# Kernel tuning notes

Hardware: AMD Instinct MI355X
Metric: run time of the kernel (lower is better)

## Reference

```python
import jax, jax.numpy as jnp
import numpy as np

N_NODES = 50000
IN_C = 128
OUT_C = 128
EDGE_F = 65
N_EDGES = 800000
EDGE_ATTR_COLS = 70


def setup_inputs() -> dict:
    key = jax.random.key(0)
    ks = jax.random.split(key, 10)
    fcat = 3 * IN_C + EDGE_F
    sc = lambda d: 1.0 / np.sqrt(d)
    return {
        "x": jax.random.normal(ks[0], (N_NODES, IN_C), dtype=jnp.float32),
        "edge_index": jax.random.randint(ks[1], (2, N_EDGES), 0, N_NODES, dtype=jnp.int32),
        "edge_attr": jax.random.normal(ks[2], (N_EDGES, EDGE_ATTR_COLS), dtype=jnp.float32),
        # f_linear: Linear(fcat -> IN_C, bias=True) followed by ELU
        "Wf": jax.random.normal(ks[3], (fcat, IN_C), dtype=jnp.float32) * sc(fcat),
        "bf": jnp.zeros((IN_C,), dtype=jnp.float32),
        # q/k linears: Linear(IN_C -> IN_C, bias=False)
        "Wq": jax.random.normal(ks[4], (IN_C, IN_C), dtype=jnp.float32) * sc(IN_C),
        "Wk": jax.random.normal(ks[5], (IN_C, IN_C), dtype=jnp.float32) * sc(IN_C),
        # alinear: Linear(IN_C -> 1, bias=False) + Tanh
        "Wa": jax.random.normal(ks[6], (IN_C, 1), dtype=jnp.float32) * sc(IN_C),
        # updatalinear: Linear(IN_C -> OUT_C, bias=True)
        "Wu": jax.random.normal(ks[7], (IN_C, OUT_C), dtype=jnp.float32) * sc(IN_C),
        "bu": jnp.zeros((OUT_C,), dtype=jnp.float32),
    }


def reference(x, edge_index, edge_attr, Wf, bf, Wq, Wk, Wa, Wu, bu):
    src = edge_index[0]
    tgt = edge_index[1]
    # message: gather endpoints, concat with delta and edge features, fuse MLP
    ni = x[src]                      # [E, C]
    nj = x[tgt]                      # [E, C]
    mask = (edge_attr[:, 0:1] < 8).astype(x.dtype)  # [E, 1]
    fcat = jnp.concatenate([ni, nj, ni - nj, edge_attr[:, :EDGE_F]], axis=1)
    f = jax.nn.elu(fcat @ Wf + bf) * mask           # [E, C]
    scale = IN_C ** (-0.5)
    q = ni @ Wq                                      # [E, C]
    k = f @ Wk                                       # [E, C]
    a = jnp.tanh((q * k * scale) @ Wa)               # [E, 1]
    # NOTE: faithful to source: denominator = exp(sum(a)), not sum(exp(a))
    numerator = jnp.exp(a)
    a_sum = jax.ops.segment_sum(a, src, num_segments=N_NODES)   # [N, 1]
    denominator = jnp.exp(a_sum)[src]                            # [E, 1]
    s = numerator / denominator
    z = s * f                                        # [E, C]
    # aggregate: scatter-sum over source nodes
    aggr = jax.ops.segment_sum(z, src, num_segments=N_NODES)     # [N, C]
    # update
    return (x + aggr) @ Wu + bu
```

## Files before the change

### kernel.cpp

```cpp
#include <hip/hip_runtime.h>

#define E_EDGES 800000
#define NN 50000
#define C 128
#define EAC 70
#define EF 65
#define NB 196
#define SCALE 0.08838834764831845f

typedef __attribute__((ext_vector_type(8))) short short8;
typedef __attribute__((ext_vector_type(4))) float floatx4;

__device__ __forceinline__ unsigned short f2bf(float f) {
  unsigned u = __builtin_bit_cast(unsigned, f);
  unsigned r = (u + 0x7FFFu + ((u >> 16) & 1u)) >> 16;
  return (unsigned short)r;
}
__device__ __forceinline__ float bf2f(unsigned short h) {
  unsigned u = ((unsigned)h) << 16;
  return __builtin_bit_cast(float, u);
}

__device__ __forceinline__ float fast_tanh(float x) {
  float xc = fminf(fmaxf(x, -15.f), 15.f);
  float t = __expf(2.f * xc);
  return (t - 1.f) * __builtin_amdgcn_rcpf(t + 1.f);
}
__device__ __forceinline__ float fast_elu(float v) {
  return v > 0.f ? v : (__expf(v) - 1.f);
}

__device__ __forceinline__ void atomic_pk_add_bf16(unsigned short* p, float lo, float hi) {
  unsigned pk = (unsigned)f2bf(lo) | ((unsigned)f2bf(hi) << 16);
  asm volatile("global_atomic_pk_add_bf16 %0, %1, off"
               :: "v"((unsigned long long)(uintptr_t)p), "v"(pk) : "memory");
}

__global__ void setup_kernel(const float* __restrict__ Wf, const float* __restrict__ Wq,
                             const float* __restrict__ Wk, const float* __restrict__ Wa,
                             const int* __restrict__ src, unsigned short* __restrict__ wfrag,
                             float* __restrict__ Wm, int* __restrict__ deg) {
  int b = blockIdx.x;
  if (b < 64) {
    int idx = b * 256 + threadIdx.x;
    int r = idx >> 7, d = idx & 127;
    const float* wq = Wq + (size_t)r * C;
    const float* wk = Wk + (size_t)d * C;
    float s = 0.f;
    for (int c = 0; c < C; ++c) s += wq[c] * Wa[c] * wk[c];
    Wm[idx] = s * SCALE;
  } else if (b < 240) {
    int idx = (b - 64) * 256 + threadIdx.x;
    int arr = idx >> 14;
    int rem = idx & 16383;
    int j = rem & 7;
    int l = (rem >> 3) & 63;
    int st = rem >> 9;
    int s = st >> 3, t = st & 7;
    int k = s * 32 + (l >> 4) * 8 + j;
    int n = t * 16 + (l & 15);
    float v;
    if (arr == 0)      v = Wf[k * C + n] + Wf[(256 + k) * C + n];
    else if (arr == 1) v = Wf[(128 + k) * C + n] - Wf[(256 + k) * C + n];
    else               v = (k < EF) ? Wf[(384 + k) * C + n] : 0.f;
    wfrag[idx] = f2bf(v);
  } else {
    int e = (b - 240) * 256 + threadIdx.x;
    atomicAdd(deg + src[e], 1);
  }
}

__global__ __launch_bounds__(256) void m_kernel(const float* __restrict__ x,
                                                const float* __restrict__ Wm,
                                                unsigned short* __restrict__ M,
                                                unsigned short* __restrict__ XB) {
  __shared__ float rows[32][129];
  int b0 = blockIdx.x * 32;
  for (int idx = threadIdx.x; idx < 32 * 128; idx += 256) {
    int r = idx >> 7, i = idx & 127;
    int n = b0 + r;
    float v = 0.f;
    if (n < NN) {
      v = x[(size_t)n * C + i];
      XB[(size_t)n * C + i] = f2bf(v);
    }
    rows[r][i] = v;
  }
  __syncthreads();
  int tr = threadIdx.x >> 4;
  int tc = threadIdx.x & 15;
  floatx4 a00 = (floatx4){0,0,0,0}, a01 = a00, a10 = a00, a11 = a00;
  for (int i = 0; i < C; ++i) {
    float r0 = rows[tr * 2][i], r1 = rows[tr * 2 + 1][i];
    const floatx4* wr = (const floatx4*)(Wm + (size_t)i * C + tc * 8);
    floatx4 w0 = wr[0], w1 = wr[1];
    a00 += w0 * r0; a01 += w1 * r0;
    a10 += w0 * r1; a11 += w1 * r1;
  }
  int n0 = b0 + tr * 2;
  for (int rr = 0; rr < 2; ++rr) {
    int n = n0 + rr;
    if (n < NN) {
      floatx4 v0 = rr ? a10 : a00, v1 = rr ? a11 : a01;
      short8 o;
      for (int j = 0; j < 4; ++j) { o[j] = (short)f2bf(v0[j]); o[4 + j] = (short)f2bf(v1[j]); }
      *(short8*)(M + (size_t)n * C + tc * 8) = o;
    }
  }
}

__global__ __launch_bounds__(256) void scan1_kernel(const int* __restrict__ deg,
                                                    int* __restrict__ offs,
                                                    int* __restrict__ bsum) {
  __shared__ int buf[256];
  int t = threadIdx.x, n = blockIdx.x * 256 + t;
  int d = (n < NN) ? deg[n] : 0;
  buf[t] = d;
  __syncthreads();
  for (int s = 1; s < 256; s <<= 1) {
    int add = (t >= s) ? buf[t - s] : 0;
    __syncthreads();
    buf[t] += add;
    __syncthreads();
  }
  if (n < NN) offs[n] = buf[t] - d;
  if (t == 255) bsum[blockIdx.x] = buf[255];
}

__global__ __launch_bounds__(256) void scan2_kernel(const int* __restrict__ bsum,
                                                    int* __restrict__ bbase) {
  __shared__ int buf[256];
  int t = threadIdx.x;
  int d = (t < NB) ? bsum[t] : 0;
  buf[t] = d;
  __syncthreads();
  for (int s = 1; s < 256; s <<= 1) {
    int add = (t >= s) ? buf[t - s] : 0;
    __syncthreads();
    buf[t] += add;
    __syncthreads();
  }
  if (t < NB) bbase[t] = buf[t] - d;
}

__global__ void pos_kernel(const int* __restrict__ src, const int* __restrict__ tgt,
                           const int* __restrict__ offs, const int* __restrict__ bbase,
                           int* __restrict__ cursor, int4* __restrict__ rec) {
  int e = blockIdx.x * 256 + threadIdx.x;
  int r = src[e];
  int p = offs[r] + bbase[r >> 8] + atomicAdd(cursor + r, 1);
  rec[p] = make_int4(r, tgt[e], e, 0);
}

__global__ __launch_bounds__(256, 5) void edge_kernel(
    const unsigned short* __restrict__ XB, const float* __restrict__ ea,
    const float* __restrict__ bfv, const unsigned short* __restrict__ wfrag,
    const int4* __restrict__ rec, const unsigned short* __restrict__ M,
    unsigned short* __restrict__ Pb, float* __restrict__ a_sum) {
  __shared__ unsigned short f_lds[4][16][136];
  __shared__ float mask_lds[4][16];
  __shared__ float2 acf_lds[4][16];
  __shared__ int src_lds[4][16];
  const int l = threadIdx.x & 63;
  const int w = threadIdx.x >> 6;
  const int lo = l & 15, quad = l >> 4;
  const int e0 = (blockIdx.x * 4 + w) * 16;

  const short8* WF1 = (const short8*)wfrag;
  const short8* WF2 = (const short8*)(wfrag + 16384);
  const short8* WF4 = (const short8*)(wfrag + 32768);

  int p = e0 + lo;
  int4 rp = rec[p];
  int sp = rp.x, tp = rp.y, ep = rp.z;
  if (l < 16) src_lds[w][l] = sp;

  short8 niF[4], njF[4], eaF[3];
  {
    const short8* xr = (const short8*)(XB + (size_t)sp * C);
    const short8* yr = (const short8*)(XB + (size_t)tp * C);
    for (int s = 0; s < 4; ++s) { niF[s] = xr[s * 4 + quad]; njF[s] = yr[s * 4 + quad]; }
  }
  {
    const float* er = ea + (size_t)ep * EAC;
    const float2* ca = (const float2*)(er + quad * 8);
    const float2* cb = (const float2*)(er + 32 + quad * 8);
    float2 a0 = ca[0], a1 = ca[1], a2 = ca[2], a3 = ca[3];
    float2 b0 = cb[0], b1 = cb[1], b2 = cb[2], b3 = cb[3];
    short8 t0, t1, t2;
    t0[0] = (short)f2bf(a0.x); t0[1] = (short)f2bf(a0.y);
    t0[2] = (short)f2bf(a1.x); t0[3] = (short)f2bf(a1.y);
    t0[4] = (short)f2bf(a2.x); t0[5] = (short)f2bf(a2.y);
    t0[6] = (short)f2bf(a3.x); t0[7] = (short)f2bf(a3.y);
    t1[0] = (short)f2bf(b0.x); t1[1] = (short)f2bf(b0.y);
    t1[2] = (short)f2bf(b1.x); t1[3] = (short)f2bf(b1.y);
    t1[4] = (short)f2bf(b2.x); t1[5] = (short)f2bf(b2.y);
    t1[6] = (short)f2bf(b3.x); t1[7] = (short)f2bf(b3.y);
    for (int j = 0; j < 8; ++j) t2[j] = 0;
    if (quad == 0) {
      t2[0] = (short)f2bf(er[64]);
      mask_lds[w][lo] = (a0.x < 8.f) ? 1.f : 0.f;
    }
    eaF[0] = t0; eaF[1] = t1; eaF[2] = t2;
  }

  float maskv[4];
  int srcRow[4];
  for (int i = 0; i < 4; ++i) {
    maskv[i] = mask_lds[w][quad * 4 + i];
    srcRow[i] = src_lds[w][quad * 4 + i];
  }

  for (int t = 0; t < 8; ++t) {
    floatx4 acc = (floatx4){0.f, 0.f, 0.f, 0.f};
    for (int s = 0; s < 4; ++s)
      acc = __builtin_amdgcn_mfma_f32_16x16x32_bf16(niF[s], WF1[(s * 8 + t) * 64 + l], acc, 0, 0, 0);
    for (int s = 0; s < 4; ++s)
      acc = __builtin_amdgcn_mfma_f32_16x16x32_bf16(njF[s], WF2[(s * 8 + t) * 64 + l], acc, 0, 0, 0);
    for (int s = 0; s < 3; ++s)
      acc = __builtin_amdgcn_mfma_f32_16x16x32_bf16(eaF[s], WF4[(s * 8 + t) * 64 + l], acc, 0, 0, 0);
    float bias = bfv[lo + 16 * t];
    for (int i = 0; i < 4; ++i) {
      float v = fast_elu(acc[i] + bias);
      v *= maskv[i];
      f_lds[w][quad * 4 + i][lo + 16 * t] = f2bf(v);
    }
  }

  for (int i = 0; i < 4; ++i) {
    const short8 fv = *(const short8*)&f_lds[w][quad * 4 + i][lo * 8];
    const short8 mv = *(const short8*)(M + (size_t)srcRow[i] * C + lo * 8);
    float d = 0.f;
    for (int j = 0; j < 8; ++j)
      d += bf2f((unsigned short)fv[j]) * bf2f((unsigned short)mv[j]);
    d += __shfl_xor(d, 1);
    d += __shfl_xor(d, 2);
    d += __shfl_xor(d, 4);
    d += __shfl_xor(d, 8);
    float a = fast_tanh(d);
    if (lo == 0) acf_lds[w][quad * 4 + i] = make_float2(a, __expf(a));
  }

  {
    const int col = l << 1;
    float acc0 = 0.f, acc1 = 0.f, accA = 0.f;
    int cur = __builtin_amdgcn_readfirstlane(src_lds[w][0]);
#pragma unroll
    for (int r = 0; r < 16; ++r) {
      int s_r = __builtin_amdgcn_readfirstlane(src_lds[w][r]);
      if (s_r != cur) {
        atomic_pk_add_bf16(Pb + (size_t)cur * C + col, acc0, acc1);
        if (l == 0) atomicAdd(a_sum + cur, accA);
        acc0 = acc1 = accA = 0.f;
        cur = s_r;
      }
      unsigned v = *(const unsigned*)&f_lds[w][r][col];
      float2 acf = acf_lds[w][r];
      acc0 = fmaf(acf.y, bf2f((unsigned short)(v & 0xFFFFu)), acc0);
      acc1 = fmaf(acf.y, bf2f((unsigned short)(v >> 16)), acc1);
      accA += acf.x;
    }
    atomic_pk_add_bf16(Pb + (size_t)cur * C + col, acc0, acc1);
    if (l == 0) atomicAdd(a_sum + cur, accA);
  }
}

__global__ __launch_bounds__(256) void node_kernel(
    const float* __restrict__ x, const unsigned short* __restrict__ Pb,
    const float* __restrict__ a_sum, const float* __restrict__ Wu,
    const float* __restrict__ bu, float* __restrict__ out) {
  __shared__ float rows[32][129];
  int b0 = blockIdx.x * 32;
  for (int idx = threadIdx.x; idx < 32 * 128; idx += 256) {
    int r = idx >> 7, i = idx & 127;
    int n = b0 + r;
    float v = 0.f;
    if (n < NN) v = x[(size_t)n * C + i] + __expf(-a_sum[n]) * bf2f(Pb[(size_t)n * C + i]);
    rows[r][i] = v;
  }
  __syncthreads();
  int tr = threadIdx.x >> 4;
  int tc = threadIdx.x & 15;
  floatx4 a00 = (floatx4){0,0,0,0}, a01 = a00, a10 = a00, a11 = a00;
  for (int i = 0; i < C; ++i) {
    float r0 = rows[tr * 2][i], r1 = rows[tr * 2 + 1][i];
    const floatx4* wr = (const floatx4*)(Wu + (size_t)i * C + tc * 8);
    floatx4 w0 = wr[0], w1 = wr[1];
    a00 += w0 * r0; a01 += w1 * r0;
    a10 += w0 * r1; a11 += w1 * r1;
  }
  const floatx4* bv = (const floatx4*)(bu + tc * 8);
  floatx4 bb0 = bv[0], bb1 = bv[1];
  int n0 = b0 + tr * 2;
  if (n0 < NN) {
    floatx4* o = (floatx4*)(out + (size_t)n0 * C + tc * 8);
    o[0] = a00 + bb0; o[1] = a01 + bb1;
  }
  if (n0 + 1 < NN) {
    floatx4* o = (floatx4*)(out + (size_t)(n0 + 1) * C + tc * 8);
    o[0] = a10 + bb0; o[1] = a11 + bb1;
  }
}

__global__ __launch_bounds__(256, 4) void fb_edge_kernel(
    const float* __restrict__ x, const int* __restrict__ src,
    const int* __restrict__ tgt, const float* __restrict__ ea,
    const float* __restrict__ bfv, const unsigned short* __restrict__ wfrag,
    const unsigned short* __restrict__ M, float* __restrict__ a_sum,
    float* __restrict__ P) {
  __shared__ unsigned short f_lds[4][16][136];
  __shared__ float mask_lds[4][16];
  const int l = threadIdx.x & 63;
  const int w = threadIdx.x >> 6;
  const int lo = l & 15, quad = l >> 4;
  const int e0 = (blockIdx.x * 4 + w) * 16;
  const short8* WF1 = (const short8*)wfrag;
  const short8* WF2 = (const short8*)(wfrag + 16384);
  const short8* WF4 = (const short8*)(wfrag + 32768);

  int p = e0 + lo;
  int sp = src[p], tp = tgt[p];
  short8 niF[4], njF[4], eaF[3];
  {
    const float* xr = x + (size_t)sp * C;
    const float* yr = x + (size_t)tp * C;
    for (int s = 0; s < 4; ++s) {
      int kb = s * 32 + quad * 8;
      const floatx4* xv = (const floatx4*)(xr + kb);
      const floatx4* yv = (const floatx4*)(yr + kb);
      floatx4 x0 = xv[0], x1 = xv[1], y0 = yv[0], y1 = yv[1];
      short8 a, b;
      for (int j = 0; j < 4; ++j) { a[j] = (short)f2bf(x0[j]); a[4 + j] = (short)f2bf(x1[j]); }
      for (int j = 0; j < 4; ++j) { b[j] = (short)f2bf(y0[j]); b[4 + j] = (short)f2bf(y1[j]); }
      niF[s] = a; njF[s] = b;
    }
    const float* er = ea + (size_t)p * EAC;
    const float2* ca = (const float2*)(er + quad * 8);
    const float2* cb = (const float2*)(er + 32 + quad * 8);
    float2 a0 = ca[0], a1 = ca[1], a2 = ca[2], a3 = ca[3];
    float2 b0 = cb[0], b1 = cb[1], b2 = cb[2], b3 = cb[3];
    short8 t0, t1, t2;
    t0[0] = (short)f2bf(a0.x); t0[1] = (short)f2bf(a0.y);
    t0[2] = (short)f2bf(a1.x); t0[3] = (short)f2bf(a1.y);
    t0[4] = (short)f2bf(a2.x); t0[5] = (short)f2bf(a2.y);
    t0[6] = (short)f2bf(a3.x); t0[7] = (short)f2bf(a3.y);
    t1[0] = (short)f2bf(b0.x); t1[1] = (short)f2bf(b0.y);
    t1[2] = (short)f2bf(b1.x); t1[3] = (short)f2bf(b1.y);
    t1[4] = (short)f2bf(b2.x); t1[5] = (short)f2bf(b2.y);
    t1[6] = (short)f2bf(b3.x); t1[7] = (short)f2bf(b3.y);
    for (int j = 0; j < 8; ++j) t2[j] = 0;
    if (quad == 0) {
      t2[0] = (short)f2bf(er[64]);
      mask_lds[w][lo] = (a0.x < 8.f) ? 1.f : 0.f;
    }
    eaF[0] = t0; eaF[1] = t1; eaF[2] = t2;
  }
  float maskv[4];
  int srcRow[4];
  for (int i = 0; i < 4; ++i) {
    maskv[i] = mask_lds[w][quad * 4 + i];
    srcRow[i] = src[e0 + quad * 4 + i];
  }
  for (int t = 0; t < 8; ++t) {
    floatx4 acc = (floatx4){0.f, 0.f, 0.f, 0.f};
    for (int s = 0; s < 4; ++s)
      acc = __builtin_amdgcn_mfma_f32_16x16x32_bf16(niF[s], WF1[(s * 8 + t) * 64 + l], acc, 0, 0, 0);
    for (int s = 0; s < 4; ++s)
      acc = __builtin_amdgcn_mfma_f32_16x16x32_bf16(njF[s], WF2[(s * 8 + t) * 64 + l], acc, 0, 0, 0);
    for (int s = 0; s < 3; ++s)
      acc = __builtin_amdgcn_mfma_f32_16x16x32_bf16(eaF[s], WF4[(s * 8 + t) * 64 + l], acc, 0, 0, 0);
    float bias = bfv[lo + 16 * t];
    for (int i = 0; i < 4; ++i) {
      float v = fast_elu(acc[i] + bias);
      v *= maskv[i];
      f_lds[w][quad * 4 + i][lo + 16 * t] = f2bf(v);
    }
  }
  for (int i = 0; i < 4; ++i) {
    const short8 fv = *(const short8*)&f_lds[w][quad * 4 + i][lo * 8];
    const short8 mv = *(const short8*)(M + (size_t)srcRow[i] * C + lo * 8);
    float d = 0.f;
    for (int j = 0; j < 8; ++j)
      d += bf2f((unsigned short)fv[j]) * bf2f((unsigned short)mv[j]);
    d += __shfl_xor(d, 1);
    d += __shfl_xor(d, 2);
    d += __shfl_xor(d, 4);
    d += __shfl_xor(d, 8);
    float a = fast_tanh(d);
    float cf = __expf(a);
    if (lo == 0) atomicAdd(a_sum + srcRow[i], a);
    float* Prow = P + (size_t)srcRow[i] * C;
    for (int j = 0; j < 8; ++j)
      atomicAdd(Prow + lo * 8 + j, cf * bf2f((unsigned short)fv[j]));
  }
}

__global__ __launch_bounds__(256) void fb_node_kernel(
    const float* __restrict__ x, const float* __restrict__ P,
    const float* __restrict__ a_sum, const float* __restrict__ Wu,
    const float* __restrict__ bu, float* __restrict__ out) {
  __shared__ float rows[32][129];
  int b0 = blockIdx.x * 32;
  for (int idx = threadIdx.x; idx < 32 * 128; idx += 256) {
    int r = idx >> 7, i = idx & 127;
    int n = b0 + r;
    float v = 0.f;
    if (n < NN) v = x[(size_t)n * C + i] + expf(-a_sum[n]) * P[(size_t)n * C + i];
    rows[r][i] = v;
  }
  __syncthreads();
  int tr = threadIdx.x >> 4;
  int tc = threadIdx.x & 15;
  floatx4 a00 = (floatx4){0,0,0,0}, a01 = a00, a10 = a00, a11 = a00;
  for (int i = 0; i < C; ++i) {
    float r0 = rows[tr * 2][i], r1 = rows[tr * 2 + 1][i];
    const floatx4* wr = (const floatx4*)(Wu + (size_t)i * C + tc * 8);
    floatx4 w0 = wr[0], w1 = wr[1];
    a00 += w0 * r0; a01 += w1 * r0;
    a10 += w0 * r1; a11 += w1 * r1;
  }
  const floatx4* bv = (const floatx4*)(bu + tc * 8);
  floatx4 bb0 = bv[0], bb1 = bv[1];
  int n0 = b0 + tr * 2;
  if (n0 < NN) {
    floatx4* o = (floatx4*)(out + (size_t)n0 * C + tc * 8);
    o[0] = a00 + bb0; o[1] = a01 + bb1;
  }
  if (n0 + 1 < NN) {
    floatx4* o = (floatx4*)(out + (size_t)(n0 + 1) * C + tc * 8);
    o[0] = a10 + bb0; o[1] = a11 + bb1;
  }
}

extern "C" void kernel_launch(void* const* d_in, const int* in_sizes, int n_in,
                              void* d_out, int out_size, void* d_ws, size_t ws_size,
                              hipStream_t stream) {
  const float* x  = (const float*)d_in[0];
  const int*   ei = (const int*)d_in[1];
  const float* ea = (const float*)d_in[2];
  const float* Wf = (const float*)d_in[3];
  const float* bf = (const float*)d_in[4];
  const float* Wq = (const float*)d_in[5];
  const float* Wk = (const float*)d_in[6];
  const float* Wa = (const float*)d_in[7];
  const float* Wu = (const float*)d_in[8];
  const float* bu = (const float*)d_in[9];
  float* out = (float*)d_out;
  const int* src = ei;
  const int* tgt = ei + E_EDGES;

  size_t off = 0;
  auto take = [&](size_t n) { size_t r = off; off += (n + 255) & ~(size_t)255; return r; };
  size_t oP    = take((size_t)NN * C * 2);
  size_t oAs   = take((size_t)NN * 4);
  size_t oDeg  = take((size_t)NN * 4);
  size_t oCur  = take((size_t)NN * 4);
  size_t oOffs = take((size_t)NN * 4);
  size_t oBs   = take((size_t)NB * 4);
  size_t oBb   = take((size_t)NB * 4);
  size_t oRec  = take((size_t)E_EDGES * 16);
  size_t oWfr  = take((size_t)45056 * 2);
  size_t oWm   = take((size_t)C * C * 4);
  size_t oM    = take((size_t)NN * C * 2);
  size_t oXB   = take((size_t)NN * C * 2);
  size_t need = off;

  if (ws_size >= need) {
    unsigned short* Pb = (unsigned short*)((char*)d_ws + oP);
    float* a_sum = (float*)((char*)d_ws + oAs);
    int* deg = (int*)((char*)d_ws + oDeg);
    int* cursor = (int*)((char*)d_ws + oCur);
    int* offs = (int*)((char*)d_ws + oOffs);
    int* bsum = (int*)((char*)d_ws + oBs);
    int* bbase = (int*)((char*)d_ws + oBb);
    int4* rec = (int4*)((char*)d_ws + oRec);
    unsigned short* wfrag = (unsigned short*)((char*)d_ws + oWfr);
    float* Wm = (float*)((char*)d_ws + oWm);
    unsigned short* M = (unsigned short*)((char*)d_ws + oM);
    unsigned short* XB = (unsigned short*)((char*)d_ws + oXB);

    hipMemsetAsync(Pb, 0, oOffs - oP, stream);
    setup_kernel<<<3365, 256, 0, stream>>>(Wf, Wq, Wk, Wa, src, wfrag, Wm, deg);
    m_kernel<<<(NN + 31) / 32, 256, 0, stream>>>(x, Wm, M, XB);
    scan1_kernel<<<NB, 256, 0, stream>>>(deg, offs, bsum);
    scan2_kernel<<<1, 256, 0, stream>>>(bsum, bbase);
    pos_kernel<<<E_EDGES / 256, 256, 0, stream>>>(src, tgt, offs, bbase, cursor, rec);
    edge_kernel<<<E_EDGES / 64, 256, 0, stream>>>(XB, ea, bf, wfrag, rec, M, Pb, a_sum);
    node_kernel<<<(NN + 31) / 32, 256, 0, stream>>>(x, Pb, a_sum, Wu, bu, out);
  } else {
    size_t f = 0;
    auto tk = [&](size_t n) { size_t r = f; f += (n + 255) & ~(size_t)255; return r; };
    size_t fP = tk((size_t)NN * C * 4);
    size_t fAs = tk((size_t)NN * 4);
    size_t fDeg = tk((size_t)NN * 4);
    size_t fWfr = tk((size_t)45056 * 2);
    size_t fWm = tk((size_t)C * C * 4);
    size_t fM = tk((size_t)NN * C * 2);
    float* P = (float*)((char*)d_ws + fP);
    float* a_sum = (float*)((char*)d_ws + fAs);
    int* deg = (int*)((char*)d_ws + fDeg);
    unsigned short* wfrag = (unsigned short*)((char*)d_ws + fWfr);
    float* Wm = (float*)((char*)d_ws + fWm);
    unsigned short* M = (unsigned short*)((char*)d_ws + fM);
    hipMemsetAsync(P, 0, (size_t)NN * C * 4 + 256 + NN * 4, stream);
    setup_kernel<<<3365, 256, 0, stream>>>(Wf, Wq, Wk, Wa, src, wfrag, Wm, deg);
    m_kernel<<<(NN + 31) / 32, 256, 0, stream>>>(x, Wm, M, (unsigned short*)P);
    hipMemsetAsync(P, 0, (size_t)NN * C * 4, stream);
    fb_edge_kernel<<<E_EDGES / 64, 256, 0, stream>>>(x, src, tgt, ea, bf, wfrag, M,
                                                     a_sum, P);
    fb_node_kernel<<<(NN + 31) / 32, 256, 0, stream>>>(x, P, a_sum, Wu, bu, out);
  }
}
```

Baseline: 790.5 us.

## Pre-pack bf16 edge attributes with src/tgt into sorted record in pos_kernel

```diff
diff --git a/kernel.cpp b/kernel.cpp
--- a/kernel.cpp
+++ b/kernel.cpp
@@ -144,19 +144,46 @@
 }
 
 __global__ void pos_kernel(const int* __restrict__ src, const int* __restrict__ tgt,
-                           const int* __restrict__ offs, const int* __restrict__ bbase,
-                           int* __restrict__ cursor, int4* __restrict__ rec) {
+                           const float* __restrict__ ea, const int* __restrict__ offs,
+                           const int* __restrict__ bbase, int* __restrict__ cursor,
+                           unsigned short* __restrict__ eaB) {
   int e = blockIdx.x * 256 + threadIdx.x;
   int r = src[e];
   int p = offs[r] + bbase[r >> 8] + atomicAdd(cursor + r, 1);
-  rec[p] = make_int4(r, tgt[e], e, 0);
+  const float* er = ea + (size_t)e * EAC;
+  unsigned short* o = eaB + (size_t)p * 72;
+  float v0 = 0.f;
+  short8 rcd[9];
+#pragma unroll
+  for (int s = 0; s < 8; ++s) {
+    short8 t;
+#pragma unroll
+    for (int j = 0; j < 4; ++j) {
+      float2 f = *(const float2*)(er + s * 8 + j * 2);
+      t[2 * j] = (short)f2bf(f.x);
+      t[2 * j + 1] = (short)f2bf(f.y);
+      if (s == 0 && j == 0) v0 = f.x;
+    }
+    rcd[s] = t;
+  }
+  int tg = tgt[e];
+  short8 t8;
+  t8[0] = (short)f2bf(er[64]);
+  t8[1] = (short)((v0 < 8.f) ? 0x3F80 : 0);
+  t8[2] = 0; t8[3] = 0;
+  t8[4] = (short)(r & 0xFFFF);  t8[5] = (short)(((unsigned)r) >> 16);
+  t8[6] = (short)(tg & 0xFFFF); t8[7] = (short)(((unsigned)tg) >> 16);
+  rcd[8] = t8;
+#pragma unroll
+  for (int s = 0; s < 9; ++s)
+    *(short8*)(o + s * 8) = rcd[s];
 }
 
 __global__ __launch_bounds__(256, 5) void edge_kernel(
-    const unsigned short* __restrict__ XB, const float* __restrict__ ea,
-    const float* __restrict__ bfv, const unsigned short* __restrict__ wfrag,
-    const int4* __restrict__ rec, const unsigned short* __restrict__ M,
-    unsigned short* __restrict__ Pb, float* __restrict__ a_sum) {
+    const unsigned short* __restrict__ XB, const float* __restrict__ bfv,
+    const unsigned short* __restrict__ wfrag, const unsigned short* __restrict__ eaB,
+    const unsigned short* __restrict__ M, unsigned short* __restrict__ Pb,
+    float* __restrict__ a_sum) {
   __shared__ unsigned short f_lds[4][16][136];
   __shared__ float mask_lds[4][16];
   __shared__ float2 acf_lds[4][16];
@@ -171,8 +198,9 @@
   const short8* WF4 = (const short8*)(wfrag + 32768);
 
   int p = e0 + lo;
-  int4 rp = rec[p];
-  int sp = rp.x, tp = rp.y, ep = rp.z;
+  const unsigned short* er = eaB + (size_t)p * 72;
+  int2 st = *(const int2*)(er + 68);
+  int sp = st.x, tp = st.y;
   if (l < 16) src_lds[w][l] = sp;
 
   short8 niF[4], njF[4], eaF[3];
@@ -182,26 +210,14 @@
     for (int s = 0; s < 4; ++s) { niF[s] = xr[s * 4 + quad]; njF[s] = yr[s * 4 + quad]; }
   }
   {
-    const float* er = ea + (size_t)ep * EAC;
-    const float2* ca = (const float2*)(er + quad * 8);
-    const float2* cb = (const float2*)(er + 32 + quad * 8);
-    float2 a0 = ca[0], a1 = ca[1], a2 = ca[2], a3 = ca[3];
-    float2 b0 = cb[0], b1 = cb[1], b2 = cb[2], b3 = cb[3];
-    short8 t0, t1, t2;
-    t0[0] = (short)f2bf(a0.x); t0[1] = (short)f2bf(a0.y);
-    t0[2] = (short)f2bf(a1.x); t0[3] = (short)f2bf(a1.y);
-    t0[4] = (short)f2bf(a2.x); t0[5] = (short)f2bf(a2.y);
-    t0[6] = (short)f2bf(a3.x); t0[7] = (short)f2bf(a3.y);
-    t1[0] = (short)f2bf(b0.x); t1[1] = (short)f2bf(b0.y);
-    t1[2] = (short)f2bf(b1.x); t1[3] = (short)f2bf(b1.y);
-    t1[4] = (short)f2bf(b2.x); t1[5] = (short)f2bf(b2.y);
-    t1[6] = (short)f2bf(b3.x); t1[7] = (short)f2bf(b3.y);
+    eaF[0] = *(const short8*)(er + quad * 8);
+    eaF[1] = *(const short8*)(er + 32 + quad * 8);
+    ushort2 mm = *(const ushort2*)(er + 64);
+    short8 t2;
     for (int j = 0; j < 8; ++j) t2[j] = 0;
-    if (quad == 0) {
-      t2[0] = (short)f2bf(er[64]);
-      mask_lds[w][lo] = (a0.x < 8.f) ? 1.f : 0.f;
-    }
-    eaF[0] = t0; eaF[1] = t1; eaF[2] = t2;
+    t2[0] = (short)mm.x;
+    eaF[2] = t2;
+    if (quad == 0) mask_lds[w][lo] = bf2f(mm.y);
   }
 
   float maskv[4];
@@ -458,7 +474,7 @@
   size_t oOffs = take((size_t)NN * 4);
   size_t oBs   = take((size_t)NB * 4);
   size_t oBb   = take((size_t)NB * 4);
-  size_t oRec  = take((size_t)E_EDGES * 16);
+  size_t oEaB  = take((size_t)E_EDGES * 144);
   size_t oWfr  = take((size_t)45056 * 2);
   size_t oWm   = take((size_t)C * C * 4);
   size_t oM    = take((size_t)NN * C * 2);
@@ -473,7 +489,7 @@
     int* offs = (int*)((char*)d_ws + oOffs);
     int* bsum = (int*)((char*)d_ws + oBs);
     int* bbase = (int*)((char*)d_ws + oBb);
-    int4* rec = (int4*)((char*)d_ws + oRec);
+    unsigned short* eaB = (unsigned short*)((char*)d_ws + oEaB);
     unsigned short* wfrag = (unsigned short*)((char*)d_ws + oWfr);
     float* Wm = (float*)((char*)d_ws + oWm);
     unsigned short* M = (unsigned short*)((char*)d_ws + oM);
@@ -484,8 +500,8 @@
     m_kernel<<<(NN + 31) / 32, 256, 0, stream>>>(x, Wm, M, XB);
     scan1_kernel<<<NB, 256, 0, stream>>>(deg, offs, bsum);
     scan2_kernel<<<1, 256, 0, stream>>>(bsum, bbase);
-    pos_kernel<<<E_EDGES / 256, 256, 0, stream>>>(src, tgt, offs, bbase, cursor, rec);
-    edge_kernel<<<E_EDGES / 64, 256, 0, stream>>>(XB, ea, bf, wfrag, rec, M, Pb, a_sum);
+    pos_kernel<<<E_EDGES / 256, 256, 0, stream>>>(src, tgt, ea, offs, bbase, cursor, eaB);
+    edge_kernel<<<E_EDGES / 64, 256, 0, stream>>>(XB, bf, wfrag, eaB, M, Pb, a_sum);
     node_kernel<<<(NN + 31) / 32, 256, 0, stream>>>(x, Pb, a_sum, Wu, bu, out);
   } else {
     size_t f = 0;
```

Result: slower. 836.7 us (+5.9%).
